# Performance work log

Measured on AMD Instinct MI355X. Metric: run time of the kernel, lower is better.

## Reference

```python
import jax, jax.numpy as jnp
import numpy as np

B, NF, FD = 2048, 64, 32   # batch, n_features, feature_dim
S = NF // 2                # n_sites
D, OD = 32, 32             # bond_dim, out_dim


def setup_inputs() -> dict:
    key = jax.random.key(0)
    k1, k2, k3, k4 = jax.random.split(key, 4)
    sc = 1.0 / np.sqrt(FD * D)
    x = jax.random.normal(k1, (B, NF, FD), dtype=jnp.float32)
    L = jax.random.normal(k2, (S, FD, D, D), dtype=jnp.float32) * sc
    R = jax.random.normal(k3, (S, FD, D, D), dtype=jnp.float32) * sc
    O = jax.random.normal(k4, (S, D, D, OD), dtype=jnp.float32) * sc
    bias = jnp.zeros((S, OD), dtype=jnp.float32)
    return {"x": x, "L": L, "R": R, "O": O, "bias": bias}


def reference(x, L, R, O, bias):
    # x: [B, 2*S, FD] -> left/right features per site
    xL = x[:, 0::2, :]  # [B, S, FD]
    xR = x[:, 1::2, :]  # [B, S, FD]
    # feature -> bond matrices
    A = jnp.einsum('bsf,sfam->bsam', xL, L)   # [B, S, D, D]
    Bm = jnp.einsum('bsg,sgan->bsan', xR, R)  # [B, S, D, D]
    # contract shared bond leg a, then output tensor
    M = jnp.einsum('bsam,bsan->bsmn', A, Bm)  # [B, S, D, D]
    out = jnp.einsum('bsmn,smno->bso', M, O)  # [B, S, OD]
    return out + bias  # bias broadcast over batch; activation is None
```

## Files before the change

### kernel.cpp

```cpp
#include <hip/hip_runtime.h>
#include <hip/hip_bf16.h>

typedef __attribute__((ext_vector_type(4)))  _Float16 h4;
typedef __attribute__((ext_vector_type(8)))  _Float16 h8;
typedef __attribute__((ext_vector_type(4)))  float f32x4;
typedef __attribute__((ext_vector_type(16))) float f32x16;

__global__ __launch_bounds__(64) void conv_kernel(
    const float* __restrict__ Rg, const float* __restrict__ Og,
    _Float16* __restrict__ Rb, _Float16* __restrict__ Op)
{
    __shared__ float tile[32][33];
    const int which = blockIdx.y;
    const int s = blockIdx.x >> 5, q = blockIdx.x & 31;
    const int t = threadIdx.x, tl = t & 31, th = t >> 5;

    if (which == 0) {
        #pragma unroll
        for (int j = 0; j < 16; ++j) {
            int ar = 2*j + th;
            tile[tl][ar] = Rg[(((size_t)s*32 + q)*32 + ar)*32 + tl];
        }
        __syncthreads();
        #pragma unroll
        for (int j = 0; j < 16; ++j) {
            int nr = 2*j + th;
            Rb[(((size_t)s*32 + q)*32 + nr)*32 + tl] = (_Float16)tile[nr][tl];
        }
    } else {
        #pragma unroll
        for (int j = 0; j < 16; ++j) {
            int nr = 2*j + th;
            tile[tl][nr] = Og[(((size_t)s*32 + q)*32 + nr)*32 + tl];
        }
        __syncthreads();
        #pragma unroll
        for (int j = 0; j < 16; ++j) {
            int orow = 2*j + th;
            Op[((size_t)s*32 + orow)*1024 + q*32 + tl] = (_Float16)tile[orow][tl];
        }
    }
}

__global__ __launch_bounds__(256) void tmake_kernel(
    const float* __restrict__ Lg, const _Float16* __restrict__ Rb,
    const _Float16* __restrict__ Op, _Float16* __restrict__ Tp)
{
    __shared__ __align__(16) char Wl[65536];
    __shared__ float Ltile[32][33];
    __shared__ __align__(16) char Opc[8192];

    const int bid = blockIdx.x;
    const int s = bid & 31, f = bid >> 5;
    const int t = threadIdx.x, wid = t >> 6, l = t & 63;
    const int llo = l & 15, lhi = l >> 4;

    #pragma unroll
    for (int i = 0; i < 4; ++i) {
        int idx = i*256 + t, a = idx >> 5, m = idx & 31;
        Ltile[a][m] = Lg[(((size_t)s*32 + f)*32 + a)*32 + m];
    }
    __syncthreads();

    h8 afrag[2];
    #pragma unroll
    for (int mt = 0; mt < 2; ++mt)
        #pragma unroll
        for (int j = 0; j < 8; ++j)
            afrag[mt][j] = (_Float16)Ltile[8*lhi + j][mt*16 + llo];

    const _Float16* Rbs = Rb + (size_t)s*32768;
    const _Float16* Ops = Op + (size_t)s*32768;

    #pragma unroll 4
    for (int nt = 0; nt < 16; ++nt) {
        int col = (wid*16 + nt)*16 + llo;
        h8 bfrag = *(const h8*)(Rbs + col*32 + 8*lhi);
        int g = col >> 5, n = col & 31;
        #pragma unroll
        for (int mt = 0; mt < 2; ++mt) {
            f32x4 c = __builtin_amdgcn_mfma_f32_16x16x32_f16(afrag[mt], bfrag, (f32x4)(0.0f), 0, 0, 0);
            #pragma unroll
            for (int r = 0; r < 4; ++r) {
                int m = mt*16 + 4*lhi + r;
                int byte = (g*2048 + (m*32 + n)*2) ^ ((g & 7) << 4);
                *(_Float16*)(Wl + byte) = (_Float16)c[r];
            }
        }
    }
    __syncthreads();

    const int gt = wid >> 1, ot = wid & 1;
    const int grow = gt*16 + llo;
    const int orow = ot*16 + llo;
    f32x4 acc = (f32x4)(0.0f);
    for (int c = 0; c < 8; ++c) {
        {
            int o = t >> 3, j = t & 7;
            uint4 v0 = *(const uint4*)(Ops + o*1024 + c*128 + j*8);
            uint4 v1 = *(const uint4*)(Ops + o*1024 + c*128 + (j+8)*8);
            *(uint4*)(Opc + ((o*256 + j*16)     ^ ((o & 7) << 4))) = v0;
            *(uint4*)(Opc + ((o*256 + (j+8)*16) ^ ((o & 7) << 4))) = v1;
        }
        __syncthreads();
        #pragma unroll
        for (int ksl = 0; ksl < 4; ++ksl) {
            int ks = c*4 + ksl;
            int abyte = (grow*2048 + ks*64 + lhi*16) ^ ((grow & 7) << 4);
            h8 af = *(const h8*)(Wl + abyte);
            h8 bf = *(const h8*)(Opc + ((orow*256 + ksl*64 + lhi*16) ^ ((orow & 7) << 4)));
            acc = __builtin_amdgcn_mfma_f32_16x16x32_f16(af, bf, acc, 0, 0, 0);
        }
        __syncthreads();
    }
    _Float16* Tps = Tp + (size_t)s*32768;
    h4 res;
    #pragma unroll
    for (int r = 0; r < 4; ++r) res[r] = (_Float16)acc[r];
    *(h4*)(Tps + ((f*2 + gt)*32 + orow)*16 + 4*lhi) = res;
}

__global__ __launch_bounds__(256) void main_kernel(
    const float* __restrict__ x, const _Float16* __restrict__ Tp,
    const float* __restrict__ bias, float* __restrict__ out)
{
    __shared__ __align__(16) char To2[65536];
    __shared__ __align__(16) char xl2[16384];
    __shared__ __align__(16) char xr2[16384];

    const int bid = blockIdx.x;
    const int s = bid & 31;
    const int b0 = (bid >> 5) * 256;
    const int t = threadIdx.x;
    const int l = t & 63, wid = t >> 6;
    const int lo5 = l & 31, hi = l >> 5;

    const char* Tps = (const char*)(Tp + (size_t)s*32768);

    uint4 tv[4];
    #pragma unroll
    for (int r = 0; r < 4; ++r)
        tv[r] = *(const uint4*)(Tps + r*4096 + t*16);

    #pragma unroll
    for (int i = 0; i < 16; ++i) {
        int idx = i*256 + t, b = idx >> 4, c = idx & 15;
        float4 v = *(const float4*)(x + (size_t)(b0 + b)*2048 + s*64 + c*4);
        h4 w; w[0] = (_Float16)v.x; w[1] = (_Float16)v.y;
              w[2] = (_Float16)v.z; w[3] = (_Float16)v.w;
        if (c < 8) *(h4*)(xl2 + (c >> 1)*4096 + b*16 + (c & 1)*8) = w;
        else { int c2 = c - 8; *(h4*)(xr2 + (c2 >> 1)*4096 + b*16 + (c2 & 1)*8) = w; }
    }
    #pragma unroll
    for (int r = 0; r < 4; ++r)
        *(uint4*)(To2 + r*4096 + t*16) = tv[r];
    __syncthreads();

    const int sub0 = wid*2;
    h8 xlr_[2][4];
    h8 xrr_[2][2];
    #pragma unroll
    for (int sb = 0; sb < 2; ++sb) {
        int b = (sub0 + sb)*32 + lo5;
        #pragma unroll
        for (int blk = 0; blk < 4; ++blk)
            xlr_[sb][blk] = *(const h8*)(xl2 + blk*4096 + b*16);
        #pragma unroll
        for (int gh = 0; gh < 2; ++gh)
            xrr_[sb][gh] = *(const h8*)(xr2 + (gh*2 + hi)*4096 + b*16);
    }

    f32x16 acc0 = (f32x16)(0.0f), acc1 = (f32x16)(0.0f);

    #pragma unroll
    for (int c = 0; c < 4; ++c) {
        if (c < 3) {
            #pragma unroll
            for (int r = 0; r < 4; ++r)
                tv[r] = *(const uint4*)(Tps + (c + 1)*16384 + r*4096 + t*16);
        }
        #pragma unroll
        for (int ksl = 0; ksl < 16; ++ksl) {
            int ks = c*16 + ksl;
            int f = ks >> 1, gh = ks & 1;
            h8 bf = *(const h8*)(To2 + ks*1024 + lo5*32 + hi*16);
            _Float16 xs0 = xlr_[0][f >> 3][f & 7];
            h8 z0 = xrr_[0][gh] * xs0;
            acc0 = __builtin_amdgcn_mfma_f32_32x32x16_f16(z0, bf, acc0, 0, 0, 0);
            _Float16 xs1 = xlr_[1][f >> 3][f & 7];
            h8 z1 = xrr_[1][gh] * xs1;
            acc1 = __builtin_amdgcn_mfma_f32_32x32x16_f16(z1, bf, acc1, 0, 0, 0);
        }
        if (c < 3) {
            #pragma unroll
            for (int r = 0; r < 4; ++r)
                *(uint4*)(To2 + (c + 1)*16384 + r*4096 + t*16) = tv[r];
            __syncthreads();
        }
    }

    const float bv = bias[s*32 + lo5];
    #pragma unroll
    for (int r = 0; r < 16; ++r) {
        int rowoff = (r & 3) + 8*(r >> 2) + 4*hi;
        out[(size_t)(b0 + sub0*32 + rowoff)*1024 + s*32 + lo5] = acc0[r] + bv;
        out[(size_t)(b0 + sub0*32 + 32 + rowoff)*1024 + s*32 + lo5] = acc1[r] + bv;
    }
}

extern "C" void kernel_launch(void* const* d_in, const int* in_sizes, int n_in,
                              void* d_out, int out_size, void* d_ws, size_t ws_size,
                              hipStream_t stream) {
    const float* x    = (const float*)d_in[0];
    const float* L    = (const float*)d_in[1];
    const float* R    = (const float*)d_in[2];
    const float* O    = (const float*)d_in[3];
    const float* bias = (const float*)d_in[4];
    float* out = (float*)d_out;

    _Float16* Rb = (_Float16*)d_ws;
    _Float16* Op = Rb + 1048576;
    _Float16* Tp = Op + 1048576;

    conv_kernel<<<dim3(1024, 2), 64, 0, stream>>>(R, O, Rb, Op);
    tmake_kernel<<<dim3(1024), 256, 0, stream>>>(L, Rb, Op, Tp);
    main_kernel<<<dim3(256), 256, 0, stream>>>(x, Tp, bias, out);
}
```

Before: 34.58 us.

## Split K across waves, halve main tiles, and pre-layout O for tmake

The main kernel now handles 128 batch rows per block instead of 256 and launches twice as many blocks. It double-buffers T in smaller LDS tiles and splits the K loop between wave pairs, adding a cross-wave reduction through LDS. The tmake kernel reads O from a pre-packed fragment layout straight from global memory, which removes the staged LDS loop and its barriers. It also swaps the MFMA operand roles so each lane writes packed h4 stores under a new XOR swizzle, and splits K across waves with a reduction. conv_kernel emits vectorized fp16 stores in the new layouts, and launch bounds request higher occupancy, at the cost of extra reduction traffic and barriers.

```diff
diff --git a/kernel.cpp b/kernel.cpp
--- a/kernel.cpp
+++ b/kernel.cpp
@@ -8,11 +8,11 @@
 
 __global__ __launch_bounds__(64) void conv_kernel(
     const float* __restrict__ Rg, const float* __restrict__ Og,
-    _Float16* __restrict__ Rb, _Float16* __restrict__ Op)
+    _Float16* __restrict__ Rb, char* __restrict__ Opp)
 {
     __shared__ float tile[32][33];
-    const int which = blockIdx.y;
-    const int s = blockIdx.x >> 5, q = blockIdx.x & 31;
+    const int bid = blockIdx.x;
+    const int s = bid & 31, q = (bid >> 5) & 31, which = bid >> 10;
     const int t = threadIdx.x, tl = t & 31, th = t >> 5;
 
     if (which == 0) {
@@ -22,10 +22,14 @@
             tile[tl][ar] = Rg[(((size_t)s*32 + q)*32 + ar)*32 + tl];
         }
         __syncthreads();
-        #pragma unroll
-        for (int j = 0; j < 16; ++j) {
-            int nr = 2*j + th;
-            Rb[(((size_t)s*32 + q)*32 + nr)*32 + tl] = (_Float16)tile[nr][tl];
+        _Float16* dst = Rb + ((size_t)s*32 + q)*1024;
+        #pragma unroll
+        for (int it = 0; it < 4; ++it) {
+            int nr = it*8 + (t >> 3), a0 = (t & 7)*4;
+            h4 w;
+            #pragma unroll
+            for (int k = 0; k < 4; ++k) w[k] = (_Float16)tile[nr][a0 + k];
+            *(h4*)(dst + nr*32 + a0) = w;
         }
     } else {
         #pragma unroll
@@ -34,177 +38,206 @@
             tile[tl][nr] = Og[(((size_t)s*32 + q)*32 + nr)*32 + tl];
         }
         __syncthreads();
-        #pragma unroll
-        for (int j = 0; j < 16; ++j) {
-            int orow = 2*j + th;
-            Op[((size_t)s*32 + orow)*1024 + q*32 + tl] = (_Float16)tile[orow][tl];
-        }
-    }
-}
-
-__global__ __launch_bounds__(256) void tmake_kernel(
+        char* dst = Opp + (size_t)s*65536 + q*2048;
+        int o = t & 31, cq = t >> 5;
+        #pragma unroll
+        for (int it = 0; it < 2; ++it) {
+            int c = it*2 + cq;
+            h8 w;
+            #pragma unroll
+            for (int k = 0; k < 8; ++k) w[k] = (_Float16)tile[o][c*8 + k];
+            *(h8*)(dst + c*512 + o*16) = w;
+        }
+    }
+}
+
+__global__ __launch_bounds__(256, 2) void tmake_kernel(
     const float* __restrict__ Lg, const _Float16* __restrict__ Rb,
-    const _Float16* __restrict__ Op, _Float16* __restrict__ Tp)
+    const char* __restrict__ Opp, char* __restrict__ Tp)
 {
     __shared__ __align__(16) char Wl[65536];
-    __shared__ float Ltile[32][33];
-    __shared__ __align__(16) char Opc[8192];
-
     const int bid = blockIdx.x;
     const int s = bid & 31, f = bid >> 5;
     const int t = threadIdx.x, wid = t >> 6, l = t & 63;
     const int llo = l & 15, lhi = l >> 4;
 
-    #pragma unroll
-    for (int i = 0; i < 4; ++i) {
-        int idx = i*256 + t, a = idx >> 5, m = idx & 31;
-        Ltile[a][m] = Lg[(((size_t)s*32 + f)*32 + a)*32 + m];
-    }
-    __syncthreads();
-
-    h8 afrag[2];
+    const float* Lsf = Lg + ((size_t)s*32 + f)*1024;
+    h8 bfr[2];
     #pragma unroll
     for (int mt = 0; mt < 2; ++mt)
         #pragma unroll
         for (int j = 0; j < 8; ++j)
-            afrag[mt][j] = (_Float16)Ltile[8*lhi + j][mt*16 + llo];
+            bfr[mt][j] = (_Float16)Lsf[(8*lhi + j)*32 + mt*16 + llo];
 
     const _Float16* Rbs = Rb + (size_t)s*32768;
-    const _Float16* Ops = Op + (size_t)s*32768;
 
     #pragma unroll 4
     for (int nt = 0; nt < 16; ++nt) {
-        int col = (wid*16 + nt)*16 + llo;
-        h8 bfrag = *(const h8*)(Rbs + col*32 + 8*lhi);
-        int g = col >> 5, n = col & 31;
+        int gnb = (wid*16 + nt)*16;
+        h8 af = *(const h8*)(Rbs + (gnb + llo)*32 + 8*lhi);
+        int g = gnb >> 5;
+        int nbase = (gnb & 31) + 4*lhi;
         #pragma unroll
         for (int mt = 0; mt < 2; ++mt) {
-            f32x4 c = __builtin_amdgcn_mfma_f32_16x16x32_f16(afrag[mt], bfrag, (f32x4)(0.0f), 0, 0, 0);
-            #pragma unroll
-            for (int r = 0; r < 4; ++r) {
-                int m = mt*16 + 4*lhi + r;
-                int byte = (g*2048 + (m*32 + n)*2) ^ ((g & 7) << 4);
-                *(_Float16*)(Wl + byte) = (_Float16)c[r];
-            }
-        }
-    }
-    __syncthreads();
-
-    const int gt = wid >> 1, ot = wid & 1;
-    const int grow = gt*16 + llo;
+            f32x4 d = __builtin_amdgcn_mfma_f32_16x16x32_f16(af, bfr[mt], (f32x4)(0.f), 0, 0, 0);
+            int m = mt*16 + llo;
+            h4 w;
+            #pragma unroll
+            for (int r = 0; r < 4; ++r) w[r] = (_Float16)d[r];
+            int byte = (g*2048 + m*64 + nbase*2) ^ ((((g & 7) ^ (m & 7))) << 4);
+            *(h4*)(Wl + byte) = w;
+        }
+    }
+    __syncthreads();
+
+    const int ot = wid & 1, kq = wid >> 1;
     const int orow = ot*16 + llo;
-    f32x4 acc = (f32x4)(0.0f);
-    for (int c = 0; c < 8; ++c) {
+    const char* Opps = Opp + (size_t)s*65536;
+    f32x4 acc0 = (f32x4)(0.f), acc1 = (f32x4)(0.f);
+    #pragma unroll 4
+    for (int ksl = 0; ksl < 16; ++ksl) {
+        int ks = kq*16 + ksl;
+        h8 bf = *(const h8*)(Opps + (ks*4 + lhi)*512 + orow*16);
         {
-            int o = t >> 3, j = t & 7;
-            uint4 v0 = *(const uint4*)(Ops + o*1024 + c*128 + j*8);
-            uint4 v1 = *(const uint4*)(Ops + o*1024 + c*128 + (j+8)*8);
-            *(uint4*)(Opc + ((o*256 + j*16)     ^ ((o & 7) << 4))) = v0;
-            *(uint4*)(Opc + ((o*256 + (j+8)*16) ^ ((o & 7) << 4))) = v1;
-        }
-        __syncthreads();
-        #pragma unroll
-        for (int ksl = 0; ksl < 4; ++ksl) {
-            int ks = c*4 + ksl;
-            int abyte = (grow*2048 + ks*64 + lhi*16) ^ ((grow & 7) << 4);
-            h8 af = *(const h8*)(Wl + abyte);
-            h8 bf = *(const h8*)(Opc + ((orow*256 + ksl*64 + lhi*16) ^ ((orow & 7) << 4)));
-            acc = __builtin_amdgcn_mfma_f32_16x16x32_f16(af, bf, acc, 0, 0, 0);
-        }
-        __syncthreads();
-    }
-    _Float16* Tps = Tp + (size_t)s*32768;
-    h4 res;
-    #pragma unroll
-    for (int r = 0; r < 4; ++r) res[r] = (_Float16)acc[r];
-    *(h4*)(Tps + ((f*2 + gt)*32 + orow)*16 + 4*lhi) = res;
-}
-
-__global__ __launch_bounds__(256) void main_kernel(
-    const float* __restrict__ x, const _Float16* __restrict__ Tp,
+            int grow = llo;
+            int byte = (grow*2048 + ks*64 + lhi*16) ^ ((((grow & 7) ^ (ks & 7))) << 4);
+            h8 af = *(const h8*)(Wl + byte);
+            acc0 = __builtin_amdgcn_mfma_f32_16x16x32_f16(af, bf, acc0, 0, 0, 0);
+        }
+        {
+            int grow = 16 + llo;
+            int byte = (grow*2048 + ks*64 + lhi*16) ^ ((((grow & 7) ^ (ks & 7))) << 4);
+            h8 af = *(const h8*)(Wl + byte);
+            acc1 = __builtin_amdgcn_mfma_f32_16x16x32_f16(af, bf, acc1, 0, 0, 0);
+        }
+    }
+    __syncthreads();
+    if (kq == 1) {
+        *(f32x4*)(Wl + ((ot*2 + 0)*64 + l)*16) = acc0;
+        *(f32x4*)(Wl + ((ot*2 + 1)*64 + l)*16) = acc1;
+    }
+    __syncthreads();
+    if (kq == 0) {
+        acc0 += *(const f32x4*)(Wl + ((ot*2 + 0)*64 + l)*16);
+        acc1 += *(const f32x4*)(Wl + ((ot*2 + 1)*64 + l)*16);
+        char* Tps = Tp + (size_t)s*65536;
+        h4 w0, w1;
+        #pragma unroll
+        for (int r = 0; r < 4; ++r) { w0[r] = (_Float16)acc0[r]; w1[r] = (_Float16)acc1[r]; }
+        *(h4*)(Tps + (f*2 + 0)*1024 + orow*32 + lhi*8) = w0;
+        *(h4*)(Tps + (f*2 + 1)*1024 + orow*32 + lhi*8) = w1;
+    }
+}
+
+__global__ __launch_bounds__(256, 3) void main_kernel(
+    const float* __restrict__ x, const char* __restrict__ Tp,
     const float* __restrict__ bias, float* __restrict__ out)
 {
-    __shared__ __align__(16) char To2[65536];
-    __shared__ __align__(16) char xl2[16384];
-    __shared__ __align__(16) char xr2[16384];
+    __shared__ __align__(16) char Tb0[16384];
+    __shared__ __align__(16) char Tb1[16384];
+    __shared__ __align__(16) char xl2[8192];
+    __shared__ __align__(16) char xr2[8192];
 
     const int bid = blockIdx.x;
     const int s = bid & 31;
-    const int b0 = (bid >> 5) * 256;
-    const int t = threadIdx.x;
-    const int l = t & 63, wid = t >> 6;
+    const int b0 = (bid >> 5) * 128;
+    const int t = threadIdx.x, wid = t >> 6, l = t & 63;
     const int lo5 = l & 31, hi = l >> 5;
-
-    const char* Tps = (const char*)(Tp + (size_t)s*32768);
+    const int kh = wid & 1, sbp = wid >> 1;
+
+    const char* Tps = Tp + (size_t)s*65536;
 
     uint4 tv[4];
     #pragma unroll
-    for (int r = 0; r < 4; ++r)
-        tv[r] = *(const uint4*)(Tps + r*4096 + t*16);
-
-    #pragma unroll
-    for (int i = 0; i < 16; ++i) {
+    for (int i = 0; i < 4; ++i)
+        tv[i] = *(const uint4*)(Tps + (i*256 + t)*16);
+
+    #pragma unroll
+    for (int i = 0; i < 8; ++i) {
         int idx = i*256 + t, b = idx >> 4, c = idx & 15;
         float4 v = *(const float4*)(x + (size_t)(b0 + b)*2048 + s*64 + c*4);
         h4 w; w[0] = (_Float16)v.x; w[1] = (_Float16)v.y;
               w[2] = (_Float16)v.z; w[3] = (_Float16)v.w;
-        if (c < 8) *(h4*)(xl2 + (c >> 1)*4096 + b*16 + (c & 1)*8) = w;
-        else { int c2 = c - 8; *(h4*)(xr2 + (c2 >> 1)*4096 + b*16 + (c2 & 1)*8) = w; }
-    }
-    #pragma unroll
-    for (int r = 0; r < 4; ++r)
-        *(uint4*)(To2 + r*4096 + t*16) = tv[r];
-    __syncthreads();
-
-    const int sub0 = wid*2;
-    h8 xlr_[2][4];
-    h8 xrr_[2][2];
+        if (c < 8) *(h4*)(xl2 + (c >> 1)*2048 + b*16 + (c & 1)*8) = w;
+        else { int c2 = c - 8; *(h4*)(xr2 + (c2 >> 1)*2048 + b*16 + (c2 & 1)*8) = w; }
+    }
+    #pragma unroll
+    for (int i = 0; i < 4; ++i)
+        *(uint4*)(Tb0 + (i*256 + t)*16) = tv[i];
+    #pragma unroll
+    for (int i = 0; i < 4; ++i)
+        tv[i] = *(const uint4*)(Tps + 16384 + (i*256 + t)*16);
+    __syncthreads();
+
+    h4 xlh[2][4];
+    h8 xrh[2][2];
     #pragma unroll
     for (int sb = 0; sb < 2; ++sb) {
-        int b = (sub0 + sb)*32 + lo5;
-        #pragma unroll
-        for (int blk = 0; blk < 4; ++blk)
-            xlr_[sb][blk] = *(const h8*)(xl2 + blk*4096 + b*16);
+        int b = sbp*64 + sb*32 + lo5;
+        #pragma unroll
+        for (int c = 0; c < 4; ++c)
+            xlh[sb][c] = *(const h4*)(xl2 + c*2048 + b*16 + kh*8);
         #pragma unroll
         for (int gh = 0; gh < 2; ++gh)
-            xrr_[sb][gh] = *(const h8*)(xr2 + (gh*2 + hi)*4096 + b*16);
-    }
-
-    f32x16 acc0 = (f32x16)(0.0f), acc1 = (f32x16)(0.0f);
+            xrh[sb][gh] = *(const h8*)(xr2 + (gh*2 + hi)*2048 + b*16);
+    }
+
+    f32x16 acc0 = (f32x16)(0.f), acc1 = (f32x16)(0.f);
 
     #pragma unroll
     for (int c = 0; c < 4; ++c) {
+        const char* Tc = (c & 1) ? Tb1 : Tb0;
+        #pragma unroll
+        for (int i = 0; i < 8; ++i) {
+            int ksl = kh*8 + i;
+            h8 bf = *(const h8*)(Tc + ksl*1024 + lo5*32 + hi*16);
+            _Float16 x0 = xlh[0][c][i >> 1];
+            _Float16 x1 = xlh[1][c][i >> 1];
+            h8 z0 = xrh[0][i & 1] * x0;
+            acc0 = __builtin_amdgcn_mfma_f32_32x32x16_f16(z0, bf, acc0, 0, 0, 0);
+            h8 z1 = xrh[1][i & 1] * x1;
+            acc1 = __builtin_amdgcn_mfma_f32_32x32x16_f16(z1, bf, acc1, 0, 0, 0);
+        }
         if (c < 3) {
-            #pragma unroll
-            for (int r = 0; r < 4; ++r)
-                tv[r] = *(const uint4*)(Tps + (c + 1)*16384 + r*4096 + t*16);
-        }
-        #pragma unroll
-        for (int ksl = 0; ksl < 16; ++ksl) {
-            int ks = c*16 + ksl;
-            int f = ks >> 1, gh = ks & 1;
-            h8 bf = *(const h8*)(To2 + ks*1024 + lo5*32 + hi*16);
-            _Float16 xs0 = xlr_[0][f >> 3][f & 7];
-            h8 z0 = xrr_[0][gh] * xs0;
-            acc0 = __builtin_amdgcn_mfma_f32_32x32x16_f16(z0, bf, acc0, 0, 0, 0);
-            _Float16 xs1 = xlr_[1][f >> 3][f & 7];
-            h8 z1 = xrr_[1][gh] * xs1;
-            acc1 = __builtin_amdgcn_mfma_f32_32x32x16_f16(z1, bf, acc1, 0, 0, 0);
-        }
-        if (c < 3) {
-            #pragma unroll
-            for (int r = 0; r < 4; ++r)
-                *(uint4*)(To2 + (c + 1)*16384 + r*4096 + t*16) = tv[r];
+            char* Tn = (c & 1) ? Tb0 : Tb1;
+            #pragma unroll
+            for (int i = 0; i < 4; ++i)
+                *(uint4*)(Tn + (i*256 + t)*16) = tv[i];
+            if (c < 2) {
+                #pragma unroll
+                for (int i = 0; i < 4; ++i)
+                    tv[i] = *(const uint4*)(Tps + (c + 2)*16384 + (i*256 + t)*16);
+            }
             __syncthreads();
         }
     }
 
-    const float bv = bias[s*32 + lo5];
-    #pragma unroll
-    for (int r = 0; r < 16; ++r) {
-        int rowoff = (r & 3) + 8*(r >> 2) + 4*hi;
-        out[(size_t)(b0 + sub0*32 + rowoff)*1024 + s*32 + lo5] = acc0[r] + bv;
-        out[(size_t)(b0 + sub0*32 + 32 + rowoff)*1024 + s*32 + lo5] = acc1[r] + bv;
+    __syncthreads();
+    if (kh == 1) {
+        #pragma unroll
+        for (int rq = 0; rq < 4; ++rq) {
+            f32x4 p0, p1;
+            #pragma unroll
+            for (int rr = 0; rr < 4; ++rr) { p0[rr] = acc0[rq*4 + rr]; p1[rr] = acc1[rq*4 + rr]; }
+            *(f32x4*)(xl2 + sbp*4096 + rq*1024 + l*16) = p0;
+            *(f32x4*)(xr2 + sbp*4096 + rq*1024 + l*16) = p1;
+        }
+    }
+    __syncthreads();
+    if (kh == 0) {
+        const float bv = bias[s*32 + lo5];
+        #pragma unroll
+        for (int rq = 0; rq < 4; ++rq) {
+            f32x4 p0 = *(const f32x4*)(xl2 + sbp*4096 + rq*1024 + l*16);
+            f32x4 p1 = *(const f32x4*)(xr2 + sbp*4096 + rq*1024 + l*16);
+            #pragma unroll
+            for (int rr = 0; rr < 4; ++rr) {
+                int r = rq*4 + rr;
+                int rowoff = (r & 3) + 8*(r >> 2) + 4*hi;
+                out[(size_t)(b0 + sbp*64 + rowoff)*1024 + s*32 + lo5] = acc0[r] + p0[rr] + bv;
+                out[(size_t)(b0 + sbp*64 + 32 + rowoff)*1024 + s*32 + lo5] = acc1[r] + p1[rr] + bv;
+            }
+        }
     }
 }
 
@@ -218,11 +251,11 @@
     const float* bias = (const float*)d_in[4];
     float* out = (float*)d_out;
 
-    _Float16* Rb = (_Float16*)d_ws;
-    _Float16* Op = Rb + 1048576;
-    _Float16* Tp = Op + 1048576;
-
-    conv_kernel<<<dim3(1024, 2), 64, 0, stream>>>(R, O, Rb, Op);
-    tmake_kernel<<<dim3(1024), 256, 0, stream>>>(L, Rb, Op, Tp);
-    main_kernel<<<dim3(256), 256, 0, stream>>>(x, Tp, bias, out);
-}
+    _Float16* Rb  = (_Float16*)d_ws;
+    char*     Opp = (char*)(Rb + 1048576);
+    char*     Tp  = Opp + 2097152;
+
+    conv_kernel<<<dim3(2048), 64, 0, stream>>>(R, O, Rb, Opp);
+    tmake_kernel<<<dim3(1024), 256, 0, stream>>>(L, Rb, Opp, Tp);
+    main_kernel<<<dim3(512), 256, 0, stream>>>(x, Tp, bias, out);
+}
```

Result: no change. 33.99 us (-1.7%).
